# Kernel optimization log

Measured on AMD Instinct MI355X. Metric: run time of the kernel, lower is better.

The kernel has to match this reference:

```python
import jax, jax.numpy as jnp
import numpy as np
from jax import lax

VOCAB, EMBED_DIM, NUM_TAGS = 50000, 300, 16
BATCH, SEQ = 64, 512


def setup_inputs() -> dict:
    key = jax.random.key(0)
    k0, k1, k2, k3, k4 = jax.random.split(key, 5)
    text = jax.random.randint(k0, (BATCH, SEQ), 0, VOCAB)
    tags = jax.random.randint(k1, (BATCH, SEQ), 0, NUM_TAGS)
    embed_table = jax.random.normal(k2, (VOCAB, EMBED_DIM), jnp.float32) * 0.02
    W = jax.random.normal(k3, (EMBED_DIM, NUM_TAGS), jnp.float32) * 0.05
    b = jnp.zeros((NUM_TAGS,), jnp.float32)
    trans = jax.random.uniform(k4, (NUM_TAGS, NUM_TAGS), jnp.float32)
    return {"text": text, "tags": tags, "embed_table": embed_table, "W": W, "b": b, "trans": trans}


def crf_log_likelihood(probs, tags, lens, trans):
    # probs: [B,S,T] unary potentials; tags: [B,S] int; lens: [B]; trans: [T,T]
    B, S, T = probs.shape
    t_idx = jnp.arange(S)
    mask = (t_idx[None, :] < lens[:, None])  # [B,S] valid positions

    # --- gold sequence score ---
    unary = jnp.take_along_axis(probs, tags[..., None], axis=2)[..., 0]  # [B,S]
    unary_score = jnp.sum(unary * mask, axis=1)
    btrans = trans[tags[:, :-1], tags[:, 1:]]            # [B,S-1]
    bmask = mask[:, 1:]                                   # transition t->t+1 valid iff t+1 < len
    binary_score = jnp.sum(btrans * bmask, axis=1)

    # --- forward algorithm (log partition) ---
    alpha0 = probs[:, 0]                                  # [B,T]
    emits = jnp.moveaxis(probs[:, 1:], 0, 1)              # [S-1,B,T]
    ms = jnp.moveaxis(mask[:, 1:], 0, 1)                  # [S-1,B]

    def step(alpha, inp):
        emit, m = inp
        new = jax.nn.logsumexp(alpha[:, :, None] + trans[None, :, :], axis=1) + emit
        return jnp.where(m[:, None], new, alpha), None

    alpha, _ = lax.scan(step, alpha0, (emits, ms))
    log_norm = jax.nn.logsumexp(alpha, axis=-1)           # [B]
    return unary_score + binary_score - log_norm


def reference(text, tags, embed_table, W, b, trans):
    # dropout is identity in eval/reference mode
    text_lens = jnp.sum((text != 0).astype(jnp.int32), axis=1)  # [B]
    probs = embed_table[text] @ W + b                            # [B,S,T]
    log_likelihood = crf_log_likelihood(probs, tags, text_lens, trans)
    return probs, text_lens, log_likelihood
```

## Files before the change

kernel.cpp:

```cpp
#include <hip/hip_runtime.h>
#include <hip/hip_bf16.h>

#define VOCAB 50000
#define ED    300
#define NT    16
#define BB    64
#define SS    512

#define LOG2E 1.4426950408889634f
#define LN2   0.6931471805599453f
#define WSTR  308

__global__ __launch_bounds__(256) void probs_kernel(const int* __restrict__ text,
                                                    const float* __restrict__ emb,
                                                    const float* __restrict__ W,
                                                    const float* __restrict__ bias,
                                                    float* __restrict__ out_probs) {
  __shared__ float wt[NT * WSTR];

  const int tid = threadIdx.x;
  const int lane = tid & 63, wave = tid >> 6;
  const int r = lane >> 4, t = lane & 15;
  const int row = blockIdx.x * 16 + wave * 4 + r;

  for (int e = tid; e < ED * NT; e += 256) {
    int d = e >> 4, tt = e & 15;
    wt[tt * WSTR + d] = W[e];
  }

  const int tok = text[row];
  const float4* erow = (const float4*)(emb + (size_t)tok * ED);
  float acc = bias[t];

  float4 A[8];
#pragma unroll
  for (int i = 0; i < 8; ++i) A[i] = erow[i];

  __syncthreads();

  const float4* w4 = (const float4*)(wt + t * WSTR);
#pragma unroll
  for (int c = 0; c < 75; ++c) {
    float4 e = A[c & 7];
    if (c < 67) A[c & 7] = erow[c + 8];
    float4 w = w4[c];
    acc = fmaf(e.x, w.x, acc);
    acc = fmaf(e.y, w.y, acc);
    acc = fmaf(e.z, w.z, acc);
    acc = fmaf(e.w, w.w, acc);
  }
  out_probs[(size_t)row * NT + t] = acc;
}

template <int CTRL>
__device__ __forceinline__ float dppmov(float x) {
  int xi = __float_as_int(x);
  return __int_as_float(
      __builtin_amdgcn_update_dpp(xi, xi, CTRL, 0xF, 0xF, false));
}

__device__ __forceinline__ float max16(float x) {
  x = fmaxf(x, dppmov<0xB1>(x));
  x = fmaxf(x, dppmov<0x4E>(x));
  x = fmaxf(x, dppmov<0x141>(x));
  x = fmaxf(x, dppmov<0x140>(x));
  return x;
}

__device__ __forceinline__ float crf_step(float g, float pe, const float E[16]) {
  float gn, h, m, c, a1, a2, a3;
  asm("s_nop 1\n\t"
      "v_mov_b32_dpp %[h], %[g] row_half_mirror row_mask:0xf bank_mask:0xf\n\t"
      "v_mov_b32_dpp %[m], %[g] row_mirror row_mask:0xf bank_mask:0xf\n\t"
      "v_mul_f32 %[gn], %[g], %[e0]\n\t"
      "v_fmac_f32_dpp %[gn], %[g], %[e1] quad_perm:[1,0,3,2] row_mask:0xf bank_mask:0xf\n\t"
      "v_fmac_f32_dpp %[gn], %[g], %[e2] quad_perm:[2,3,0,1] row_mask:0xf bank_mask:0xf\n\t"
      "v_fmac_f32_dpp %[gn], %[g], %[e3] quad_perm:[3,2,1,0] row_mask:0xf bank_mask:0xf\n\t"
      "v_mov_b32_dpp %[c], %[m] row_half_mirror row_mask:0xf bank_mask:0xf\n\t"
      "v_mul_f32 %[a1], %[h], %[e7]\n\t"
      "v_fmac_f32_dpp %[a1], %[h], %[e6] quad_perm:[1,0,3,2] row_mask:0xf bank_mask:0xf\n\t"
      "v_fmac_f32_dpp %[a1], %[h], %[e5] quad_perm:[2,3,0,1] row_mask:0xf bank_mask:0xf\n\t"
      "v_fmac_f32_dpp %[a1], %[h], %[e4] quad_perm:[3,2,1,0] row_mask:0xf bank_mask:0xf\n\t"
      "v_mul_f32 %[a2], %[m], %[e15]\n\t"
      "v_fmac_f32_dpp %[a2], %[m], %[e14] quad_perm:[1,0,3,2] row_mask:0xf bank_mask:0xf\n\t"
      "v_fmac_f32_dpp %[a2], %[m], %[e13] quad_perm:[2,3,0,1] row_mask:0xf bank_mask:0xf\n\t"
      "v_fmac_f32_dpp %[a2], %[m], %[e12] quad_perm:[3,2,1,0] row_mask:0xf bank_mask:0xf\n\t"
      "v_mul_f32 %[a3], %[c], %[e8]\n\t"
      "v_fmac_f32_dpp %[a3], %[c], %[e9] quad_perm:[1,0,3,2] row_mask:0xf bank_mask:0xf\n\t"
      "v_fmac_f32_dpp %[a3], %[c], %[e10] quad_perm:[2,3,0,1] row_mask:0xf bank_mask:0xf\n\t"
      "v_fmac_f32_dpp %[a3], %[c], %[e11] quad_perm:[3,2,1,0] row_mask:0xf bank_mask:0xf\n\t"
      "v_add_f32 %[gn], %[gn], %[a1]\n\t"
      "v_add_f32 %[a2], %[a2], %[a3]\n\t"
      "v_add_f32 %[gn], %[gn], %[a2]\n\t"
      "v_mul_f32 %[gn], %[gn], %[pe]"
      : [gn] "=&v"(gn), [h] "=&v"(h), [m] "=&v"(m), [c] "=&v"(c),
        [a1] "=&v"(a1), [a2] "=&v"(a2), [a3] "=&v"(a3)
      : [g] "v"(g), [pe] "v"(pe),
        [e0] "v"(E[0]), [e1] "v"(E[1]), [e2] "v"(E[2]), [e3] "v"(E[3]),
        [e4] "v"(E[4]), [e5] "v"(E[5]), [e6] "v"(E[6]), [e7] "v"(E[7]),
        [e8] "v"(E[8]), [e9] "v"(E[9]), [e10] "v"(E[10]), [e11] "v"(E[11]),
        [e12] "v"(E[12]), [e13] "v"(E[13]), [e14] "v"(E[14]), [e15] "v"(E[15]));
  return gn;
}

__global__ __launch_bounds__(256) void seg_kernel(const int* __restrict__ text,
                                                  const float* __restrict__ trans,
                                                  const float* __restrict__ probs,
                                                  float* __restrict__ gm,
                                                  float* __restrict__ scl) {
  __shared__ float pe_lds[128 * 16];
  __shared__ float xsc[4][16 * 17];

  const int tid = threadIdx.x;
  const int lane = tid & 63;
  const int w = tid >> 6;
  const int q = lane >> 4;
  const int j = lane & 15;
  const int b = blockIdx.x >> 2;
  const int q4 = blockIdx.x & 3;
  const int seg = q4 * 4 + w;
  const int s_start = 1 + 32 * seg;
  const int segsz = (seg == 15) ? 31 : 32;

  {
    const float4* src = (const float4*)(probs + (size_t)b * SS * NT + (1 + 128 * q4) * NT);
    float4* dst = (float4*)pe_lds;
#pragma unroll
    for (int i = 0; i < 2; ++i) {
      float4 v = src[tid + 256 * i];
      v.x = exp2f(v.x * LOG2E);
      v.y = exp2f(v.y * LOG2E);
      v.z = exp2f(v.z * LOG2E);
      v.w = exp2f(v.w * LOG2E);
      dst[tid + 256 * i] = v;
    }
  }

  const int* tx = text + b * SS;
  int cz = 0;
#pragma unroll
  for (int k = 0; k < 8; ++k) cz += (tx[lane + 64 * k] != 0) ? 1 : 0;
  for (int off = 32; off > 0; off >>= 1) cz += __shfl_xor(cz, off, 64);
  const int len = cz;

  float E[16];
#pragma unroll
  for (int k = 0; k < 16; ++k) E[k] = __expf(trans[((j ^ k) << 4) + j]) * 0.03125f;

  __syncthreads();

  float g0 = (j == 4 * q + 0) ? 1.f : 0.f;
  float g1 = (j == 4 * q + 1) ? 1.f : 0.f;
  float g2 = (j == 4 * q + 2) ? 1.f : 0.f;
  float g3 = (j == 4 * q + 3) ? 1.f : 0.f;

  int na = len - s_start;
  na = (na < 0) ? 0 : ((na > segsz) ? segsz : na);

  const int row0 = 32 * w;
  for (int it = 0; it < na; ++it) {
    float pe = pe_lds[(row0 + it) * NT + j];
    g0 = crf_step(g0, pe, E);
    g1 = crf_step(g1, pe, E);
    g2 = crf_step(g2, pe, E);
    g3 = crf_step(g3, pe, E);
  }

  float mx = fmaxf(fmaxf(g0, g1), fmaxf(g2, g3));
  mx = max16(mx);
  mx = fmaxf(mx, __shfl_xor(mx, 16, 64));
  mx = fmaxf(mx, __shfl_xor(mx, 32, 64));
  float rr = 1.0f / mx;
  g0 *= rr; g1 *= rr; g2 *= rr; g3 *= rr;

  float* xs = xsc[w];
  xs[(4 * q + 0) * 17 + j] = g0;
  xs[(4 * q + 1) * 17 + j] = g1;
  xs[(4 * q + 2) * 17 + j] = g2;
  xs[(4 * q + 3) * 17 + j] = g3;
  float* outm = gm + ((size_t)(b * 16 + seg)) * 256;
#pragma unroll
  for (int r = 0; r < 4; ++r) {
    const int m = 4 * q + r;
    outm[m * 16 + j] = xs[(j ^ m) * 17 + j];
  }
  if (lane == 0) scl[b * 16 + seg] = __log2f(mx);
}

__global__ __launch_bounds__(64) void crf2_kernel(const int* __restrict__ text,
                                                  const int* __restrict__ tags,
                                                  const float* __restrict__ trans,
                                                  const float* __restrict__ probs,
                                                  const float* __restrict__ gm,
                                                  const float* __restrict__ scl,
                                                  float* __restrict__ out_lens,
                                                  float* __restrict__ out_ll) {
  const int tid = threadIdx.x;
  const int j = tid & 15;
  const int b = blockIdx.x;

  const int* tx = text + b * SS;
  int cz = 0;
#pragma unroll
  for (int k = 0; k < 8; ++k) cz += (tx[tid + 64 * k] != 0) ? 1 : 0;
  for (int off = 32; off > 0; off >>= 1) cz += __shfl_xor(cz, off, 64);
  const int len = cz;
  if (tid == 0) out_lens[b] = (float)len;

  const int* tg = tags + b * SS;
  int tgv[8];
  float sb = 0.f;
#pragma unroll
  for (int it = 0; it < 8; ++it) {
    const int s = tid + 64 * it;
    tgv[it] = tg[s];
    if (s >= 1 && s < len) sb += trans[tg[s - 1] * 16 + tgv[it]];
  }

  const float* pb = probs + (size_t)b * SS * NT;
  const float* gb = gm + (size_t)b * 16 * 256;

  float K2 = 0.f;
#pragma unroll
  for (int k = 0; k < 16; ++k) K2 += scl[b * 16 + k];

  float g = exp2f(pb[j] * LOG2E);

  float EA[16], EB[16];
#pragma unroll
  for (int m = 0; m < 16; ++m) EA[m] = gb[m * 16 + j];

  for (int k = 0; k < 16; k += 2) {
#pragma unroll
    for (int m = 0; m < 16; ++m) EB[m] = gb[(k + 1) * 256 + m * 16 + j];
    g = crf_step(g, 1.0f, EA);
    {
      float mx = max16(g);
      float rr = 1.0f / mx;
      K2 -= __log2f(rr);
      g *= rr;
    }
    if (k < 14) {
#pragma unroll
      for (int m = 0; m < 16; ++m) EA[m] = gb[(k + 2) * 256 + m * 16 + j];
    }
    g = crf_step(g, 1.0f, EB);
    {
      float mx = max16(g);
      float rr = 1.0f / mx;
      K2 -= __log2f(rr);
      g *= rr;
    }
  }

  float su = 0.f;
#pragma unroll
  for (int it = 0; it < 8; ++it) {
    const int s = tid + 64 * it;
    if (s < len) su += pb[s * NT + tgv[it]];
  }
  float sc = su + sb;
  for (int off = 32; off > 0; off >>= 1) sc += __shfl_xor(sc, off, 64);

  const int T = (len > 0) ? len - 1 : 0;
  float x = g;
  x += dppmov<0xB1>(x);
  x += dppmov<0x4E>(x);
  x += dppmov<0x141>(x);
  x += dppmov<0x140>(x);
  float log_norm = LN2 * (K2 + 5.0f * (float)T + __log2f(x));
  if (tid == 0) out_ll[b] = sc - log_norm;
}

extern "C" void kernel_launch(void* const* d_in, const int* in_sizes, int n_in,
                              void* d_out, int out_size, void* d_ws, size_t ws_size,
                              hipStream_t stream) {
  const int* text = (const int*)d_in[0];
  const int* tags = (const int*)d_in[1];
  const float* emb = (const float*)d_in[2];
  const float* W = (const float*)d_in[3];
  const float* bias = (const float*)d_in[4];
  const float* trans = (const float*)d_in[5];

  float* out = (float*)d_out;
  float* out_probs = out;
  float* out_lens = out + BB * SS * NT;
  float* out_ll = out + BB * SS * NT + BB;

  float* gm = (float*)d_ws;
  float* scl = gm + BB * 16 * 256;

  probs_kernel<<<(BB * SS) / 16, 256, 0, stream>>>(text, emb, W, bias, out_probs);
  seg_kernel<<<BB * 4, 256, 0, stream>>>(text, trans, out_probs, gm, scl);
  crf2_kernel<<<BB, 64, 0, stream>>>(text, tags, trans, out_probs, gm, scl,
                                     out_lens, out_ll);
}
```

Before: 138.4 us.

## Fuse CRF combine into segment kernel via last-block atomic counter

Removes the separate crf2 kernel launch: each of the four segment blocks per batch row increments an atomic counter, and the last one to finish runs the cross-segment combine. Wave 0 computes the log partition while wave 1 computes the gold-path score in parallel, and the two results meet in shared memory. This saves a kernel launch and its dependency gap, at the cost of a memset launch for the counters plus fences and atomics. It relies on `len` already being computed earlier in seg_kernel.

```diff
diff --git a/kernel.cpp b/kernel.cpp
--- a/kernel.cpp
+++ b/kernel.cpp
@@ -104,12 +104,18 @@
 }
 
 __global__ __launch_bounds__(256) void seg_kernel(const int* __restrict__ text,
+                                                  const int* __restrict__ tags,
                                                   const float* __restrict__ trans,
                                                   const float* __restrict__ probs,
                                                   float* __restrict__ gm,
-                                                  float* __restrict__ scl) {
+                                                  float* __restrict__ scl,
+                                                  int* __restrict__ cnt,
+                                                  float* __restrict__ out_lens,
+                                                  float* __restrict__ out_ll) {
   __shared__ float pe_lds[128 * 16];
   __shared__ float xsc[4][16 * 17];
+  __shared__ float hand[2];
+  __shared__ int islast;
 
   const int tid = threadIdx.x;
   const int lane = tid & 63;
@@ -185,91 +191,83 @@
     outm[m * 16 + j] = xs[(j ^ m) * 17 + j];
   }
   if (lane == 0) scl[b * 16 + seg] = __log2f(mx);
-}
-
-__global__ __launch_bounds__(64) void crf2_kernel(const int* __restrict__ text,
-                                                  const int* __restrict__ tags,
-                                                  const float* __restrict__ trans,
-                                                  const float* __restrict__ probs,
-                                                  const float* __restrict__ gm,
-                                                  const float* __restrict__ scl,
-                                                  float* __restrict__ out_lens,
-                                                  float* __restrict__ out_ll) {
-  const int tid = threadIdx.x;
-  const int j = tid & 15;
-  const int b = blockIdx.x;
-
-  const int* tx = text + b * SS;
-  int cz = 0;
-#pragma unroll
-  for (int k = 0; k < 8; ++k) cz += (tx[tid + 64 * k] != 0) ? 1 : 0;
-  for (int off = 32; off > 0; off >>= 1) cz += __shfl_xor(cz, off, 64);
-  const int len = cz;
-  if (tid == 0) out_lens[b] = (float)len;
-
-  const int* tg = tags + b * SS;
-  int tgv[8];
-  float sb = 0.f;
-#pragma unroll
-  for (int it = 0; it < 8; ++it) {
-    const int s = tid + 64 * it;
-    tgv[it] = tg[s];
-    if (s >= 1 && s < len) sb += trans[tg[s - 1] * 16 + tgv[it]];
-  }
+
+  __syncthreads();
+  if (tid == 0) {
+    __threadfence();
+    int old = __hip_atomic_fetch_add(&cnt[b * 16], 1, __ATOMIC_ACQ_REL,
+                                     __HIP_MEMORY_SCOPE_AGENT);
+    islast = (old == 3) ? 1 : 0;
+  }
+  __syncthreads();
+  if (!islast) return;
+  __threadfence();
 
   const float* pb = probs + (size_t)b * SS * NT;
-  const float* gb = gm + (size_t)b * 16 * 256;
-
-  float K2 = 0.f;
-#pragma unroll
-  for (int k = 0; k < 16; ++k) K2 += scl[b * 16 + k];
-
-  float g = exp2f(pb[j] * LOG2E);
-
-  float EA[16], EB[16];
-#pragma unroll
-  for (int m = 0; m < 16; ++m) EA[m] = gb[m * 16 + j];
-
-  for (int k = 0; k < 16; k += 2) {
-#pragma unroll
-    for (int m = 0; m < 16; ++m) EB[m] = gb[(k + 1) * 256 + m * 16 + j];
-    g = crf_step(g, 1.0f, EA);
-    {
-      float mx = max16(g);
-      float rr = 1.0f / mx;
-      K2 -= __log2f(rr);
-      g *= rr;
+
+  if (w == 0) {
+    float K2 = 0.f;
+#pragma unroll
+    for (int k = 0; k < 16; ++k) K2 += scl[b * 16 + k];
+
+    const float* gb = gm + (size_t)b * 16 * 256;
+    float g = exp2f(pb[j] * LOG2E);
+
+    float EA[16], EB[16];
+#pragma unroll
+    for (int m = 0; m < 16; ++m) EA[m] = gb[m * 16 + j];
+
+    for (int k = 0; k < 16; k += 2) {
+#pragma unroll
+      for (int m = 0; m < 16; ++m) EB[m] = gb[(k + 1) * 256 + m * 16 + j];
+      g = crf_step(g, 1.0f, EA);
+      {
+        float mxv = max16(g);
+        float rv = 1.0f / mxv;
+        K2 -= __log2f(rv);
+        g *= rv;
+      }
+      if (k < 14) {
+#pragma unroll
+        for (int m = 0; m < 16; ++m) EA[m] = gb[(k + 2) * 256 + m * 16 + j];
+      }
+      g = crf_step(g, 1.0f, EB);
+      {
+        float mxv = max16(g);
+        float rv = 1.0f / mxv;
+        K2 -= __log2f(rv);
+        g *= rv;
+      }
     }
-    if (k < 14) {
-#pragma unroll
-      for (int m = 0; m < 16; ++m) EA[m] = gb[(k + 2) * 256 + m * 16 + j];
+
+    const int T = (len > 0) ? len - 1 : 0;
+    float x = g;
+    x += dppmov<0xB1>(x);
+    x += dppmov<0x4E>(x);
+    x += dppmov<0x141>(x);
+    x += dppmov<0x140>(x);
+    float log_norm = LN2 * (K2 + 5.0f * (float)T + __log2f(x));
+    if (lane == 0) hand[1] = log_norm;
+  } else if (w == 1) {
+    if (lane == 0) out_lens[b] = (float)len;
+    const int* tg = tags + b * SS;
+    float sb = 0.f, su = 0.f;
+#pragma unroll
+    for (int it = 0; it < 8; ++it) {
+      const int s = lane + 64 * it;
+      int t1 = tg[s];
+      if (s < len) {
+        su += pb[s * NT + t1];
+        if (s >= 1) sb += trans[tg[s - 1] * 16 + t1];
+      }
     }
-    g = crf_step(g, 1.0f, EB);
-    {
-      float mx = max16(g);
-      float rr = 1.0f / mx;
-      K2 -= __log2f(rr);
-      g *= rr;
-    }
-  }
-
-  float su = 0.f;
-#pragma unroll
-  for (int it = 0; it < 8; ++it) {
-    const int s = tid + 64 * it;
-    if (s < len) su += pb[s * NT + tgv[it]];
-  }
-  float sc = su + sb;
-  for (int off = 32; off > 0; off >>= 1) sc += __shfl_xor(sc, off, 64);
-
-  const int T = (len > 0) ? len - 1 : 0;
-  float x = g;
-  x += dppmov<0xB1>(x);
-  x += dppmov<0x4E>(x);
-  x += dppmov<0x141>(x);
-  x += dppmov<0x140>(x);
-  float log_norm = LN2 * (K2 + 5.0f * (float)T + __log2f(x));
-  if (tid == 0) out_ll[b] = sc - log_norm;
+    float sc = su + sb;
+    for (int off = 32; off > 0; off >>= 1) sc += __shfl_xor(sc, off, 64);
+    if (lane == 0) hand[0] = sc;
+  }
+
+  __syncthreads();
+  if (tid == 0) out_ll[b] = hand[0] - hand[1];
 }
 
 extern "C" void kernel_launch(void* const* d_in, const int* in_sizes, int n_in,
@@ -289,9 +287,10 @@
 
   float* gm = (float*)d_ws;
   float* scl = gm + BB * 16 * 256;
-
+  int* cnt = (int*)(scl + BB * 16);
+
+  hipMemsetAsync(cnt, 0, BB * 16 * sizeof(int), stream);
   probs_kernel<<<(BB * SS) / 16, 256, 0, stream>>>(text, emb, W, bias, out_probs);
-  seg_kernel<<<BB * 4, 256, 0, stream>>>(text, trans, out_probs, gm, scl);
-  crf2_kernel<<<BB, 64, 0, stream>>>(text, tags, trans, out_probs, gm, scl,
-                                     out_lens, out_ll);
-}
+  seg_kernel<<<BB * 4, 256, 0, stream>>>(text, tags, trans, out_probs, gm, scl,
+                                         cnt, out_lens, out_ll);
+}
```

After: 156.9 us. 13.3% more time.
